# Optimization experiments

Hardware: AMD Instinct MI355X
Metric: run time of the kernel (lower is better)

Reference implementation:

```python
import jax, jax.numpy as jnp
import numpy as np

T = 3          # num_node_type
B = 8          # batch
N = 512        # max_doc_len
F_IN = 256     # in_features
F_OUT = 128    # out_features
NE = 10        # num_edge_type (embedding has NE+1 rows, row 0 = padding)
ALPHA = 0.2    # leaky relu slope
NEG = -9e15    # masked-score fill, same constant as torch source


def setup_inputs() -> dict:
    key = jax.random.key(0)
    ks = jax.random.split(key, 7)
    node_rep = jax.random.normal(ks[0], (B, N, F_IN), jnp.float32)
    node_type_mask_rep = jax.random.uniform(ks[1], (T, B, N, 1), jnp.float32)
    adj = jax.random.randint(ks[2], (B, N, N), 0, NE + 1, jnp.int32)
    W = jax.random.normal(ks[3], (T, F_IN, F_OUT), jnp.float32) * 0.05
    b = jnp.zeros((T, F_OUT), jnp.float32)
    # attention vector a in R^{2F} split into halves (GAT trick): a([h_i, x2_ij]) = h_i.a1 + x2_ij.a2 + a_b
    a1 = jax.random.normal(ks[4], (F_OUT,), jnp.float32) * 0.05
    a2 = jax.random.normal(ks[5], (F_OUT,), jnp.float32) * 0.05
    a_b = jnp.zeros((), jnp.float32)
    emb = jax.random.normal(ks[6], (NE + 1, F_OUT), jnp.float32) * 0.05
    emb = emb.at[0].set(0.0)  # padding_idx=0
    return {"node_rep": node_rep, "node_type_mask_rep": node_type_mask_rep,
            "adj": adj, "W": W, "b": b, "a1": a1, "a2": a2, "a_b": a_b, "emb": emb}


def reference(node_rep, node_type_mask_rep, adj, W, b, a1, a2, a_b, emb):
    # typed projection: h = sum_t (node_rep @ W_t + b_t) * mask_t   -> (B, N, F_OUT)
    h = jnp.sum((jnp.einsum('bni,tio->tbno', node_rep, W) + b[:, None, None, :])
                * node_type_mask_rep, axis=0)
    # edge-type embeddings: (B, N, N, F_OUT)
    E = emb[adj]
    # x_2[b,i,j] = h[b,j] + E[b,i,j]
    x2 = h[:, None, :, :] + E
    # score[b,i,j] = leakyrelu(a1.h_i + a2.x2_ij + a_b)  (decomposed concat-linear)
    s = (jnp.einsum('bif,f->bi', h, a1)[:, :, None]
         + jnp.einsum('bijf,f->bij', x2, a2) + a_b)
    s = jnp.where(s > 0, s, ALPHA * s)
    s = jnp.where(adj > 0, s, jnp.float32(NEG))
    attn = jax.nn.softmax(s, axis=2)
    # weighted sum over neighbors of x_2 (NOT h), then ELU
    out = jnp.einsum('bij,bijf->bif', attn, x2)
    return jax.nn.elu(out)
```

## Files before the change

kernel.cpp:

```cpp
#include <hip/hip_runtime.h>

constexpr int kB    = 8;
constexpr int kN    = 512;
constexpr int kFIN  = 256;
constexpr int kFOUT = 128;
constexpr int kNE   = 10;
constexpr int kBN   = kB * kN;
constexpr float kALPHA = 0.2f;
constexpr float kNEG   = -9e15f;

__global__ __launch_bounds__(256) void proj_kernel(
    const float* __restrict__ node_rep,
    const float* __restrict__ mask,
    const float* __restrict__ W,
    const float* __restrict__ bias,
    const float* __restrict__ a1,
    const float* __restrict__ a2,
    const float* __restrict__ a_b,
    const float* __restrict__ emb,
    float* __restrict__ h,
    float* __restrict__ s1,
    float* __restrict__ s2,
    float* __restrict__ emb_a2)
{
    __shared__ float xs[8][kFIN];
    __shared__ float parts[3][8][kFOUT];

    const int tid  = threadIdx.x;
    const int row0 = blockIdx.x * 8;
    const int o    = tid & 127;
    const int kq   = tid >> 7;

    #pragma unroll
    for (int it = 0; it < 2; ++it) {
        const int idx = tid + it * 256;
        const int r = idx >> 6, q = idx & 63;
        *(float4*)&xs[r][q * 4] =
            *(const float4*)&node_rep[(size_t)(row0 + r) * kFIN + q * 4];
    }
    __syncthreads();

    float acc[3][8];
    #pragma unroll
    for (int t = 0; t < 3; ++t)
        #pragma unroll
        for (int r = 0; r < 8; ++r) acc[t][r] = 0.f;

    const float* Wo = W + o;
    const int k0 = kq * 128;

    float wA[3][4], wB[3][4];
    auto loadw = [&](float (&buf)[3][4], int kk) {
        #pragma unroll
        for (int t = 0; t < 3; ++t)
            #pragma unroll
            for (int c = 0; c < 4; ++c)
                buf[t][c] = Wo[(t * kFIN + kk + c) * kFOUT];
    };
    auto fmab = [&](float (&buf)[3][4], int kb) {
        float4 xv[8];
        #pragma unroll
        for (int r = 0; r < 8; ++r)
            xv[r] = *(const float4*)&xs[r][kb];
        #pragma unroll
        for (int c = 0; c < 4; ++c)
            #pragma unroll
            for (int r = 0; r < 8; ++r) {
                const float x = ((const float*)&xv[r])[c];
                acc[0][r] = fmaf(buf[0][c], x, acc[0][r]);
                acc[1][r] = fmaf(buf[1][c], x, acc[1][r]);
                acc[2][r] = fmaf(buf[2][c], x, acc[2][r]);
            }
    };

    loadw(wA, k0);
    for (int i4 = 0; i4 < 32; i4 += 2) {
        loadw(wB, k0 + (i4 + 1) * 4);
        fmab(wA, k0 + i4 * 4);
        if (i4 + 2 < 32) loadw(wA, k0 + (i4 + 2) * 4);
        fmab(wB, k0 + (i4 + 1) * 4);
    }

    if (kq == 1) {
        #pragma unroll
        for (int t = 0; t < 3; ++t)
            #pragma unroll
            for (int r = 0; r < 8; ++r)
                parts[t][r][o] = acc[t][r];
    }
    __syncthreads();

    if (kq == 0) {
        #pragma unroll
        for (int r = 0; r < 8; ++r) {
            const int row = row0 + r;
            float hv = 0.f;
            #pragma unroll
            for (int t = 0; t < 3; ++t) {
                const float s = acc[t][r] + parts[t][r][o] + bias[t * kFOUT + o];
                hv = fmaf(mask[t * kBN + row], s, hv);
            }
            h[(size_t)row * kFOUT + o] = hv;
            parts[0][r][o] = hv;
        }
    }
    __syncthreads();

    {
        const int wv = tid >> 6, lane = tid & 63;
        #pragma unroll
        for (int rr = 0; rr < 2; ++rr) {
            const int r = wv * 2 + rr;
            const float v0 = parts[0][r][lane];
            const float v1 = parts[0][r][64 + lane];
            float p1 = v0 * a1[lane] + v1 * a1[64 + lane];
            float p2 = v0 * a2[lane] + v1 * a2[64 + lane];
            #pragma unroll
            for (int off = 32; off; off >>= 1) {
                p1 += __shfl_down(p1, off);
                p2 += __shfl_down(p2, off);
            }
            if (lane == 0) {
                s1[row0 + r] = p1 + a_b[0];
                s2[row0 + r] = p2;
            }
        }
    }

    if (blockIdx.x == 0 && tid < 176) {
        const int e = tid >> 4, l = tid & 15;
        float p = 0.f;
        #pragma unroll
        for (int k8 = 0; k8 < 8; ++k8)
            p += emb[e * kFOUT + l + k8 * 16] * a2[l + k8 * 16];
        #pragma unroll
        for (int off = 8; off; off >>= 1) p += __shfl_xor(p, off);
        if (l == 0) emb_a2[e] = p;
    }
}

__global__ __launch_bounds__(256) void attn_kernel(
    const int*   __restrict__ adj,
    const float* __restrict__ emb,
    const float* __restrict__ h,
    const float* __restrict__ s1,
    const float* __restrict__ s2,
    const float* __restrict__ emb_a2g,
    float* __restrict__ out)
{
    __shared__ float sc[8][kN + 4];
    __shared__ int   adjs[8][kN];
    __shared__ float scT[kN][8];
    __shared__ float wsum[8][16];
    __shared__ float ea2[16];

    const int tid = threadIdx.x;
    const int b   = blockIdx.x >> 6;
    const int i0  = (blockIdx.x & 63) * 8;

    if (tid < 16) ea2[tid] = emb_a2g[tid];
    __syncthreads();

    const int*   adjb = adj + ((size_t)(b * kN + i0)) * kN;
    const float* s2b  = s2 + b * kN;
    #pragma unroll
    for (int it = 0; it < 4; ++it) {
        const int idx = tid + it * 256;
        const int r = idx >> 7, jq = idx & 127;
        const int4   av  = *(const int4*)&adjb[(size_t)r * kN + jq * 4];
        const float4 s2v = *(const float4*)&s2b[jq * 4];
        const float  sr  = s1[b * kN + i0 + r];
        float4 sv; float s;
        s = sr + s2v.x + ea2[av.x]; s = s > 0.f ? s : kALPHA * s; sv.x = av.x > 0 ? s : kNEG;
        s = sr + s2v.y + ea2[av.y]; s = s > 0.f ? s : kALPHA * s; sv.y = av.y > 0 ? s : kNEG;
        s = sr + s2v.z + ea2[av.z]; s = s > 0.f ? s : kALPHA * s; sv.z = av.z > 0 ? s : kNEG;
        s = sr + s2v.w + ea2[av.w]; s = s > 0.f ? s : kALPHA * s; sv.w = av.w > 0 ? s : kNEG;
        *(float4*)&sc[r][jq * 4] = sv;
        *(int4*)&adjs[r][jq * 4] = av;
    }
    __syncthreads();

    {
        const int wv = tid >> 6, lane = tid & 63;
        #pragma unroll
        for (int rr = 0; rr < 2; ++rr) {
            const int r = wv * 2 + rr;
            float v[8]; int av[8];
            #pragma unroll
            for (int k = 0; k < 8; ++k) {
                v[k]  = sc[r][lane + k * 64];
                av[k] = adjs[r][lane + k * 64];
            }
            float m = v[0];
            #pragma unroll
            for (int k = 1; k < 8; ++k) m = fmaxf(m, v[k]);
            #pragma unroll
            for (int off = 32; off; off >>= 1) m = fmaxf(m, __shfl_xor(m, off));
            float sum = 0.f;
            #pragma unroll
            for (int k = 0; k < 8; ++k) { v[k] = __expf(v[k] - m); sum += v[k]; }
            #pragma unroll
            for (int off = 32; off; off >>= 1) sum += __shfl_xor(sum, off);
            const float inv = 1.0f / sum;
            #pragma unroll
            for (int k = 0; k < 8; ++k) {
                v[k] *= inv;
                scT[lane + k * 64][r] = v[k];
            }
            #pragma unroll
            for (int e = 1; e <= kNE; ++e) {
                float p = 0.f;
                #pragma unroll
                for (int k = 0; k < 8; ++k) p += (av[k] == e) ? v[k] : 0.f;
                #pragma unroll
                for (int off = 32; off; off >>= 1) p += __shfl_xor(p, off);
                if (lane == 0) wsum[r][e] = p;
            }
        }
    }
    __syncthreads();

    const int f4l = tid & 31;
    const int rg  = (tid >> 5) & 1;
    const int js  = tid >> 6;
    const float* hb  = h + ((size_t)(b * kN + js * 128)) * kFOUT + f4l * 4;
    const float* sct = &scT[js * 128][rg * 4];

    float4 acc0 = {0,0,0,0}, acc1 = {0,0,0,0}, acc2 = {0,0,0,0}, acc3 = {0,0,0,0};
    #pragma unroll 4
    for (int jj = 0; jj < 128; ++jj) {
        const float4 w4 = *(const float4*)&sct[jj * 8];
        const float4 hv = *(const float4*)&hb[(size_t)jj * kFOUT];
        acc0.x = fmaf(w4.x, hv.x, acc0.x); acc0.y = fmaf(w4.x, hv.y, acc0.y);
        acc0.z = fmaf(w4.x, hv.z, acc0.z); acc0.w = fmaf(w4.x, hv.w, acc0.w);
        acc1.x = fmaf(w4.y, hv.x, acc1.x); acc1.y = fmaf(w4.y, hv.y, acc1.y);
        acc1.z = fmaf(w4.y, hv.z, acc1.z); acc1.w = fmaf(w4.y, hv.w, acc1.w);
        acc2.x = fmaf(w4.z, hv.x, acc2.x); acc2.y = fmaf(w4.z, hv.y, acc2.y);
        acc2.z = fmaf(w4.z, hv.z, acc2.z); acc2.w = fmaf(w4.z, hv.w, acc2.w);
        acc3.x = fmaf(w4.w, hv.x, acc3.x); acc3.y = fmaf(w4.w, hv.y, acc3.y);
        acc3.z = fmaf(w4.w, hv.z, acc3.z); acc3.w = fmaf(w4.w, hv.w, acc3.w);
    }
    __syncthreads();

    float* parts = (float*)adjs;
    {
        const int rbase = rg * 4;
        *(float4*)&parts[((js * 8) + rbase + 0) * kFOUT + f4l * 4] = acc0;
        *(float4*)&parts[((js * 8) + rbase + 1) * kFOUT + f4l * 4] = acc1;
        *(float4*)&parts[((js * 8) + rbase + 2) * kFOUT + f4l * 4] = acc2;
        *(float4*)&parts[((js * 8) + rbase + 3) * kFOUT + f4l * 4] = acc3;
    }
    __syncthreads();

    {
        const int r  = tid >> 5;
        const int fl = (tid & 31) * 4;
        float4 a = {0,0,0,0};
        #pragma unroll
        for (int p = 0; p < 4; ++p) {
            const float4 pv = *(const float4*)&parts[((p * 8) + r) * kFOUT + fl];
            a.x += pv.x; a.y += pv.y; a.z += pv.z; a.w += pv.w;
        }
        #pragma unroll
        for (int e = 1; e <= kNE; ++e) {
            const float  wv = wsum[r][e];
            const float4 ev = *(const float4*)&emb[e * kFOUT + fl];
            a.x = fmaf(wv, ev.x, a.x); a.y = fmaf(wv, ev.y, a.y);
            a.z = fmaf(wv, ev.z, a.z); a.w = fmaf(wv, ev.w, a.w);
        }
        a.x = a.x > 0.f ? a.x : expm1f(a.x);
        a.y = a.y > 0.f ? a.y : expm1f(a.y);
        a.z = a.z > 0.f ? a.z : expm1f(a.z);
        a.w = a.w > 0.f ? a.w : expm1f(a.w);
        *(float4*)&out[((size_t)(b * kN + i0 + r)) * kFOUT + fl] = a;
    }
}

extern "C" void kernel_launch(void* const* d_in, const int* in_sizes, int n_in,
                              void* d_out, int out_size, void* d_ws, size_t ws_size,
                              hipStream_t stream) {
    const float* node_rep = (const float*)d_in[0];
    const float* mask     = (const float*)d_in[1];
    const int*   adj      = (const int*)  d_in[2];
    const float* W        = (const float*)d_in[3];
    const float* bias     = (const float*)d_in[4];
    const float* a1       = (const float*)d_in[5];
    const float* a2       = (const float*)d_in[6];
    const float* a_b      = (const float*)d_in[7];
    const float* emb      = (const float*)d_in[8];
    float* out = (float*)d_out;

    float* ws     = (float*)d_ws;
    float* h      = ws;
    float* s1     = h + (size_t)kBN * kFOUT;
    float* s2     = s1 + kBN;
    float* emb_a2 = s2 + kBN;

    proj_kernel<<<kBN / 8, 256, 0, stream>>>(
        node_rep, mask, W, bias, a1, a2, a_b, emb, h, s1, s2, emb_a2);
    attn_kernel<<<kBN / 8, 256, 0, stream>>>(
        adj, emb, h, s1, s2, emb_a2, out);
}
```

Baseline: 112.9 us.

## Split projection K-loop four ways with two output columns per thread

The projection kernel now gives each thread two adjacent output columns (float2 loads of W) and splits the K dimension across four wave groups instead of two. The partial sums are reduced through a larger shared buffer. The aim is shorter per-thread K loops and wider weight loads, so the projection stage has more parallelism and latency hiding. In exchange it uses more shared memory and a three-way reduction, and it drops the explicit double-buffered weight prefetch.

New measurement: 114.3 us. Within noise of the previous version (+1.2%).

```diff
diff --git a/kernel.cpp b/kernel.cpp
--- a/kernel.cpp
+++ b/kernel.cpp
@@ -24,12 +24,12 @@
     float* __restrict__ emb_a2)
 {
     __shared__ float xs[8][kFIN];
-    __shared__ float parts[3][8][kFOUT];
+    __shared__ float parts[3][3][8][kFOUT];
 
     const int tid  = threadIdx.x;
     const int row0 = blockIdx.x * 8;
-    const int o    = tid & 127;
-    const int kq   = tid >> 7;
+    const int o0   = (tid & 63) * 2;
+    const int kq   = tid >> 6;
 
     #pragma unroll
     for (int it = 0; it < 2; ++it) {
@@ -40,53 +40,48 @@
     }
     __syncthreads();
 
-    float acc[3][8];
+    float2 acc[3][8];
     #pragma unroll
     for (int t = 0; t < 3; ++t)
         #pragma unroll
-        for (int r = 0; r < 8; ++r) acc[t][r] = 0.f;
-
-    const float* Wo = W + o;
-    const int k0 = kq * 128;
-
-    float wA[3][4], wB[3][4];
-    auto loadw = [&](float (&buf)[3][4], int kk) {
+        for (int r = 0; r < 8; ++r) acc[t][r] = {0.f, 0.f};
+
+    const float* Wo = W + o0;
+    const int k0 = kq * 64;
+
+    #pragma unroll 2
+    for (int c = 0; c < 16; ++c) {
+        const int kb = k0 + c * 4;
+        float2 w[3][4];
         #pragma unroll
         for (int t = 0; t < 3; ++t)
             #pragma unroll
-            for (int c = 0; c < 4; ++c)
-                buf[t][c] = Wo[(t * kFIN + kk + c) * kFOUT];
-    };
-    auto fmab = [&](float (&buf)[3][4], int kb) {
+            for (int cc = 0; cc < 4; ++cc)
+                w[t][cc] = *(const float2*)&Wo[(size_t)(t * kFIN + kb + cc) * kFOUT];
         float4 xv[8];
         #pragma unroll
         for (int r = 0; r < 8; ++r)
             xv[r] = *(const float4*)&xs[r][kb];
         #pragma unroll
-        for (int c = 0; c < 4; ++c)
+        for (int cc = 0; cc < 4; ++cc)
             #pragma unroll
             for (int r = 0; r < 8; ++r) {
-                const float x = ((const float*)&xv[r])[c];
-                acc[0][r] = fmaf(buf[0][c], x, acc[0][r]);
-                acc[1][r] = fmaf(buf[1][c], x, acc[1][r]);
-                acc[2][r] = fmaf(buf[2][c], x, acc[2][r]);
-            }
-    };
-
-    loadw(wA, k0);
-    for (int i4 = 0; i4 < 32; i4 += 2) {
-        loadw(wB, k0 + (i4 + 1) * 4);
-        fmab(wA, k0 + i4 * 4);
-        if (i4 + 2 < 32) loadw(wA, k0 + (i4 + 2) * 4);
-        fmab(wB, k0 + (i4 + 1) * 4);
-    }
-
-    if (kq == 1) {
+                const float x = ((const float*)&xv[r])[cc];
+                acc[0][r].x = fmaf(w[0][cc].x, x, acc[0][r].x);
+                acc[0][r].y = fmaf(w[0][cc].y, x, acc[0][r].y);
+                acc[1][r].x = fmaf(w[1][cc].x, x, acc[1][r].x);
+                acc[1][r].y = fmaf(w[1][cc].y, x, acc[1][r].y);
+                acc[2][r].x = fmaf(w[2][cc].x, x, acc[2][r].x);
+                acc[2][r].y = fmaf(w[2][cc].y, x, acc[2][r].y);
+            }
+    }
+
+    if (kq > 0) {
         #pragma unroll
         for (int t = 0; t < 3; ++t)
             #pragma unroll
             for (int r = 0; r < 8; ++r)
-                parts[t][r][o] = acc[t][r];
+                *(float2*)&parts[kq - 1][t][r][o0] = acc[t][r];
     }
     __syncthreads();
 
@@ -94,14 +89,22 @@
         #pragma unroll
         for (int r = 0; r < 8; ++r) {
             const int row = row0 + r;
-            float hv = 0.f;
+            float2 hv = {0.f, 0.f};
             #pragma unroll
             for (int t = 0; t < 3; ++t) {
-                const float s = acc[t][r] + parts[t][r][o] + bias[t * kFOUT + o];
-                hv = fmaf(mask[t * kBN + row], s, hv);
-            }
-            h[(size_t)row * kFOUT + o] = hv;
-            parts[0][r][o] = hv;
+                float sx = acc[t][r].x, sy = acc[t][r].y;
+                #pragma unroll
+                for (int s = 0; s < 3; ++s) {
+                    sx += parts[s][t][r][o0];
+                    sy += parts[s][t][r][o0 + 1];
+                }
+                const float2 bt = *(const float2*)&bias[t * kFOUT + o0];
+                const float  mt = mask[t * kBN + row];
+                hv.x = fmaf(mt, sx + bt.x, hv.x);
+                hv.y = fmaf(mt, sy + bt.y, hv.y);
+            }
+            *(float2*)&h[(size_t)row * kFOUT + o0] = hv;
+            *(float2*)&parts[0][0][r][o0] = hv;
         }
     }
     __syncthreads();
@@ -111,8 +114,8 @@
         #pragma unroll
         for (int rr = 0; rr < 2; ++rr) {
             const int r = wv * 2 + rr;
-            const float v0 = parts[0][r][lane];
-            const float v1 = parts[0][r][64 + lane];
+            const float v0 = parts[0][0][r][lane];
+            const float v1 = parts[0][0][r][64 + lane];
             float p1 = v0 * a1[lane] + v1 * a1[64 + lane];
             float p2 = v0 * a2[lane] + v1 * a2[64 + lane];
             #pragma unroll
```
